# Kernel tuning notes

Hardware: AMD Instinct MI355X
Metric: run time of the kernel (lower is better)

The kernel has to match this reference:

```python
import jax, jax.numpy as jnp
import numpy as np

B, L, D = 2, 4096, 2048
H = 8
DK = D // H   # head qk dim = 256
DV = D // H   # head v dim = 256
KCONV = 4
BT = 64       # chunk size
EPS = 1e-5


def setup_inputs() -> dict:
    key = jax.random.key(0)
    ks = jax.random.split(key, 10)
    s = 0.02  # xavier-ish init scale (gain 2**-2.5)
    return {
        "hidden_states": jax.random.normal(ks[0], (B, L, D), jnp.float32),
        "Wq": jax.random.normal(ks[1], (D, D), jnp.float32) * s,
        "Wk": jax.random.normal(ks[2], (D, D), jnp.float32) * s,
        "Wv": jax.random.normal(ks[3], (D, D), jnp.float32) * s,
        "Wb": jax.random.normal(ks[4], (H, D), jnp.float32) * s,
        "conv_q": jax.random.normal(ks[5], (D, KCONV), jnp.float32) * 0.5,
        "conv_k": jax.random.normal(ks[6], (D, KCONV), jnp.float32) * 0.5,
        "conv_v": jax.random.normal(ks[7], (D, KCONV), jnp.float32) * 0.5,
        "g_norm": jnp.ones((DV,), jnp.float32),
        "Wo": jax.random.normal(ks[8], (D, D), jnp.float32) * s,
    }


def _causal_conv_silu(x, w):
    # depthwise causal conv1d (ShortConvolution), x: [B,L,C], w: [C,K]; silu activation
    K = w.shape[1]
    xp = jnp.pad(x, ((0, 0), (K - 1, 0), (0, 0)))
    Lx = x.shape[1]
    y = xp[:, 0:Lx, :] * w[:, 0]
    for j in range(1, K):
        y = y + xp[:, j:j + Lx, :] * w[:, j]
    return jax.nn.silu(y)


def _l2norm(x):
    return x * jax.lax.rsqrt(jnp.sum(x * x, -1, keepdims=True) + 1e-6)


def _chunk_delta_rule(q, k, v, beta):
    # q,k: [B,H,L,DK], v: [B,H,L,DV], beta: [B,H,L]
    b, h, Lq, dk = q.shape
    dv = v.shape[-1]
    nc = Lq // BT
    q = q * (dk ** -0.5)
    kb = k * beta[..., None]
    vb = v * beta[..., None]
    ch = lambda x: x.reshape(b, h, nc, BT, x.shape[-1])
    qc, kc, kbc, vbc = ch(q), ch(k), ch(kb), ch(vb)
    tri_s = jnp.tril(jnp.ones((BT, BT), bool), -1)  # strictly lower
    tri = jnp.tril(jnp.ones((BT, BT), bool))        # lower incl diag
    # M = strict_lower(K_beta K^T); T = (I+M)^{-1} via unit-lower triangular solve
    M = jnp.where(tri_s, jnp.einsum('bhntd,bhnsd->bhnts', kbc, kc), 0.0)
    Lmat = jnp.eye(BT, dtype=q.dtype) + M
    W = jax.scipy.linalg.solve_triangular(Lmat, kbc, lower=True, unit_diagonal=True)  # T @ k_beta
    U = jax.scipy.linalg.solve_triangular(Lmat, vbc, lower=True, unit_diagonal=True)  # T @ v_beta

    def step(S, xs):
        q_i, k_i, w_i, u_i = xs  # each [b,h,BT,d]
        attn = jnp.where(tri, jnp.einsum('bhtd,bhsd->bhts', q_i, k_i), 0.0)
        u_new = u_i - jnp.einsum('bhtd,bhdv->bhtv', w_i, S)
        o_i = jnp.einsum('bhtd,bhdv->bhtv', q_i, S) + jnp.einsum('bhts,bhsv->bhtv', attn, u_new)
        S = S + jnp.einsum('bhtd,bhtv->bhdv', k_i, u_new)
        return S, o_i

    mv = lambda x: jnp.moveaxis(x, 2, 0)  # chunk axis to front for scan
    S0 = jnp.zeros((b, h, dk, dv), q.dtype)
    S, o = jax.lax.scan(step, S0, (mv(qc), mv(kc), mv(W), mv(U)))
    o = jnp.moveaxis(o, 0, 2).reshape(b, h, Lq, dv)
    return o, S


def reference(hidden_states, Wq, Wk, Wv, Wb, conv_q, conv_k, conv_v, g_norm, Wo):
    hs = hidden_states
    q = _causal_conv_silu(hs @ Wq.T, conv_q)
    k = _causal_conv_silu(hs @ Wk.T, conv_k)
    v = _causal_conv_silu(hs @ Wv.T, conv_v)
    tohead = lambda x: x.reshape(B, L, H, -1).transpose(0, 2, 1, 3)  # b l (h d) -> b h l d
    q, k, v = tohead(q), tohead(k), tohead(v)
    q, k = _l2norm(q), _l2norm(k)
    beta = jax.nn.sigmoid(hs @ Wb.T).transpose(0, 2, 1)  # [B,H,L]
    o, _ = _chunk_delta_rule(q, k, v, beta)
    o = o.transpose(0, 2, 1, 3)  # [B,L,H,DV]
    o = o * jax.lax.rsqrt(jnp.mean(o * o, -1, keepdims=True) + EPS) * g_norm  # per-head RMSNorm
    return o.reshape(B, L, D) @ Wo.T
```

## Files before the change

kernel.cpp:

```cpp
#include <hip/hip_runtime.h>
#include <stdint.h>

#define TOK    8192
#define LDIM   4096
#define DDIM   2048
#define NBH    16
#define DK     256
#define NCHUNK 64

typedef __attribute__((ext_vector_type(8))) short bf16x8;
typedef __attribute__((ext_vector_type(4))) float f32x4;

#define MFMA(a,b,c) __builtin_amdgcn_mfma_f32_16x16x32_bf16((a),(b),(c),0,0,0)

__device__ __forceinline__ unsigned short f2bf(float f){
  union { float f; uint32_t u; } v; v.f = f;
  uint32_t r = v.u + 0x7FFFu + ((v.u >> 16) & 1u);
  return (unsigned short)(r >> 16);
}
__device__ __forceinline__ float bf2f(unsigned short u){
  union { uint32_t u; float f; } v; v.u = ((uint32_t)u) << 16;
  return v.f;
}

typedef __attribute__((address_space(1))) unsigned int as1_u32;
typedef __attribute__((address_space(3))) unsigned int as3_u32;
__device__ __forceinline__ void gload16(const void* g, void* l){
  __builtin_amdgcn_global_load_lds((const as1_u32*)g, (as3_u32*)l, 16, 0, 0);
}

__global__ void k_guard(float* o){ if (threadIdx.x == 0) o[0] = 0.f; }

__global__ __launch_bounds__(256) void k_f2bf(const float* __restrict__ s,
                                              unsigned short* __restrict__ d, int n)
{
  int i = (blockIdx.x*256 + threadIdx.x)*4;
  if (i >= n) return;
  float4 v = *(const float4*)(s + i);
  ushort4 o; o.x=f2bf(v.x); o.y=f2bf(v.y); o.z=f2bf(v.z); o.w=f2bf(v.w);
  *(ushort4*)(d + i) = o;
}

__global__ __launch_bounds__(256) void k_beta(const float* __restrict__ hs,
                                              const float* __restrict__ Wb,
                                              float* __restrict__ beta)
{
  const long t = blockIdx.x;
  const int tid = threadIdx.x;
  float acc[8] = {0,0,0,0,0,0,0,0};
  const float* xr = hs + t*DDIM;
  for (int i = tid; i < DDIM; i += 256){
    float x = xr[i];
    #pragma unroll
    for (int h=0; h<8; h++) acc[h] += x * Wb[h*DDIM + i];
  }
  __shared__ float red[8][4];
  const int w = tid >> 6, lane = tid & 63;
  #pragma unroll
  for (int h=0; h<8; h++){
    float s = acc[h];
    #pragma unroll
    for (int off=32; off; off>>=1) s += __shfl_down(s, off, 64);
    if (lane == 0) red[h][w] = s;
  }
  __syncthreads();
  if (tid < 8){
    float s = red[tid][0]+red[tid][1]+red[tid][2]+red[tid][3];
    float bv = 1.f/(1.f + __expf(-s));
    int b = (int)(t >> 12), l = (int)(t & 4095);
    beta[((long)(b*8 + tid))*LDIM + l] = bv;
  }
}

template <bool F32OUT>
__global__ __launch_bounds__(256,2) void k_gemm_bt(
    const unsigned short* __restrict__ A, const unsigned short* __restrict__ Bw,
    void* __restrict__ Cv, int M, int N, int K)
{
  __shared__ unsigned short As[128*32];
  __shared__ unsigned short Bs[128*32];
  const int tid = threadIdx.x;
  const int w = tid >> 6, l = tid & 63;
  const int lo = l & 15, quad = l >> 4;
  const int wm = w >> 1, wn = w & 1;
  const int gx = gridDim.x;
  int id = blockIdx.y * gx + blockIdx.x;
  const int nwg = gx * gridDim.y;
  if ((nwg & 7) == 0){
    const int q8 = nwg >> 3;
    id = (id & 7) * q8 + (id >> 3);
  }
  const int bx = id % gx, by = id / gx;
  const long tm = (long)by * 128, tn = (long)bx * 128;
  const int slot0 = (w*2+0)*64 + l;
  const int slot1 = (w*2+1)*64 + l;
  const int r0 = slot0 >> 2, c0 = (slot0 & 3) * 8;
  const int r1 = slot1 >> 2, c1 = (slot1 & 3) * 8;
  const unsigned short* pA0 = A  + (tm + r0)*(long)K + c0;
  const unsigned short* pA1 = A  + (tm + r1)*(long)K + c1;
  const unsigned short* pB0 = Bw + (tn + r0)*(long)K + c0;
  const unsigned short* pB1 = Bw + (tn + r1)*(long)K + c1;
  unsigned short* lA0 = &As[slot0*8]; unsigned short* lA1 = &As[slot1*8];
  unsigned short* lB0 = &Bs[slot0*8]; unsigned short* lB1 = &Bs[slot1*8];
  f32x4 acc[4][4] = {};
  for (int k0 = 0; k0 < K; k0 += 32){
    __syncthreads();
    gload16(pA0 + k0, lA0);
    gload16(pA1 + k0, lA1);
    gload16(pB0 + k0, lB0);
    gload16(pB1 + k0, lB1);
    __syncthreads();
    bf16x8 af[4], bg[4];
    #pragma unroll
    for (int i=0;i<4;i++){
      af[i] = *(const bf16x8*)&As[(wm*64 + i*16 + lo)*32 + quad*8];
      bg[i] = *(const bf16x8*)&Bs[(wn*64 + i*16 + lo)*32 + quad*8];
    }
    #pragma unroll
    for (int mt=0; mt<4; mt++)
      #pragma unroll
      for (int nt=0; nt<4; nt++)
        acc[mt][nt] = MFMA(af[mt], bg[nt], acc[mt][nt]);
  }
  #pragma unroll
  for (int mt=0; mt<4; mt++)
    #pragma unroll
    for (int nt=0; nt<4; nt++)
      #pragma unroll
      for (int r=0; r<4; r++){
        long m = tm + wm*64 + mt*16 + quad*4 + r;
        long n = tn + wn*64 + nt*16 + lo;
        if (F32OUT) ((float*)Cv)[m*N + n] = acc[mt][nt][r];
        else ((unsigned short*)Cv)[m*N + n] = f2bf(acc[mt][nt][r]);
      }
}

__global__ __launch_bounds__(256) void k_conv(
  const unsigned short* __restrict__ X, const float* __restrict__ Wc,
  const float* __restrict__ beta,
  unsigned short* __restrict__ O, int mode)
{
  const int lt = blockIdx.x, bh = blockIdx.y;
  const int b = bh >> 3, h = bh & 7;
  const int d = threadIdx.x;
  const int ch = h*256 + d;
  const int l0 = lt*64;
  const unsigned short* xp = X + (long)b*LDIM*DDIM + ch;
  const float4 wv = *(const float4*)(Wc + ch*4);
  float x0=0.f, x1=0.f, x2=0.f;
  if (l0 >= 3){
    x0 = bf2f(xp[(long)(l0-3)*DDIM]);
    x1 = bf2f(xp[(long)(l0-2)*DDIM]);
    x2 = bf2f(xp[(long)(l0-1)*DDIM]);
  }
  float y[64];
  #pragma unroll
  for (int i=0;i<64;i++){
    float x3 = bf2f(xp[(long)(l0+i)*DDIM]);
    float s = x0*wv.x + x1*wv.y + x2*wv.z + x3*wv.w;
    y[i] = s / (1.f + __expf(-s));
    x0 = x1; x1 = x2; x2 = x3;
  }
  unsigned short* op = O + (long)bh*LDIM*DK + d;
  if (mode == 2){
    const float* bet = beta + (long)bh*LDIM + l0;
    #pragma unroll
    for (int i=0;i<64;i++) op[(long)(l0+i)*DK] = f2bf(y[i]*bet[i]);
    return;
  }
  __shared__ float red[64*4];
  __shared__ float scl[64];
  const int wv_i = threadIdx.x >> 6, lane = threadIdx.x & 63;
  #pragma unroll
  for (int i=0;i<64;i++){
    float ss = y[i]*y[i];
    #pragma unroll
    for (int off=32; off; off>>=1) ss += __shfl_down(ss, off, 64);
    if (lane == 0) red[i*4 + wv_i] = ss;
  }
  __syncthreads();
  if (threadIdx.x < 64){
    int i = threadIdx.x;
    float s = red[i*4]+red[i*4+1]+red[i*4+2]+red[i*4+3];
    scl[i] = rsqrtf(s + 1e-6f) * (mode==0 ? 0.0625f : 1.f);
  }
  __syncthreads();
  #pragma unroll
  for (int i=0;i<64;i++) op[(long)(l0+i)*DK] = f2bf(y[i]*scl[i]);
}

__global__ __launch_bounds__(256) void k_transpose(
  const unsigned short* __restrict__ kH, unsigned short* __restrict__ kT)
{
  const int lt = blockIdx.x, dt = blockIdx.y, bh = blockIdx.z;
  __shared__ unsigned short tk[64][72];
  const int tid = threadIdx.x;
  const int rl = tid >> 2, c0 = (tid & 3) * 16;
  const long base = ((long)bh*LDIM + lt*64 + rl)*DK + dt*64 + c0;
  *(bf16x8*)&tk[rl][c0]   = *(const bf16x8*)(kH + base);
  *(bf16x8*)&tk[rl][c0+8] = *(const bf16x8*)(kH + base + 8);
  __syncthreads();
  const int rd = tid >> 2, lc0 = (tid & 3) * 16;
  bf16x8 ok0, ok1;
  #pragma unroll
  for (int j=0;j<16;j++){
    unsigned short kraw = tk[lc0+j][rd];
    if (j < 8) ok0[j] = (short)kraw; else ok1[j-8] = (short)kraw;
  }
  const long ob = ((long)bh*DK + dt*64 + rd)*LDIM + lt*64 + lc0;
  *(bf16x8*)(kT + ob) = ok0; *(bf16x8*)(kT + ob + 8) = ok1;
}

__global__ __launch_bounds__(256) void k_passA(
  const unsigned short* __restrict__ qH, const unsigned short* __restrict__ kH,
  const unsigned short* vbH,
  const unsigned short* __restrict__ kT,
  const float* __restrict__ beta,
  unsigned short* Wout,
  unsigned short* __restrict__ Uout,
  unsigned short* __restrict__ Aout)
{
  const int c = blockIdx.x, bh = blockIdx.y;
  __shared__ unsigned short Nn[64*72];
  __shared__ unsigned short NT[64*72];
  __shared__ unsigned short Pb[64*72];
  __shared__ unsigned short vT[256*72];
  const int tid = threadIdx.x;
  const int w = tid >> 6, l = tid & 63, lo = l & 15, quad = l >> 4;
  const long tokBase = (long)bh*LDIM + c*64;
  const unsigned short* qrow = qH + tokBase*DK;
  const unsigned short* krow = kH + tokBase*DK;
  const float bv = beta[tokBase + w*16 + lo];

  {
    const int r = tid >> 2, cs = (tid & 3) * 64;
    const unsigned short* vrow = vbH + (tokBase + r)*DK + cs;
    bf16x8 vv[8];
    #pragma unroll
    for (int j=0;j<8;j++) vv[j] = *(const bf16x8*)(vrow + j*8);
    #pragma unroll
    for (int j=0;j<8;j++)
      #pragma unroll
      for (int e=0;e<8;e++)
        vT[(cs + j*8 + e)*72 + r] = (unsigned short)vv[j][e];
  }

  f32x4 mAcc[4] = {}; f32x4 aAcc[4] = {};
  #pragma unroll
  for (int ks=0; ks<8; ks++){
    bf16x8 kf[4];
    #pragma unroll
    for (int nt=0; nt<4; nt++)
      kf[nt] = *(const bf16x8*)&krow[(nt*16+lo)*DK + ks*32 + quad*8];
    bf16x8 qf  = *(const bf16x8*)&qrow[(w*16+lo)*DK + ks*32 + quad*8];
    bf16x8 kfw = *(const bf16x8*)&krow[(w*16+lo)*DK + ks*32 + quad*8];
    bf16x8 kbf;
    #pragma unroll
    for (int j=0;j<8;j++) kbf[j] = (short)f2bf(bf2f((unsigned short)kfw[j]) * bv);
    #pragma unroll
    for (int nt=0; nt<4; nt++){
      mAcc[nt] = MFMA(kbf, kf[nt], mAcc[nt]);
      aAcc[nt] = MFMA(qf,  kf[nt], aAcc[nt]);
    }
  }
  unsigned short* Ap = Aout + ((long)bh*NCHUNK + c)*64*64;
  #pragma unroll
  for (int nt=0; nt<4; nt++)
    #pragma unroll
    for (int r=0; r<4; r++){
      int t = w*16 + quad*4 + r, s = nt*16 + lo;
      float mv = (t > s) ? mAcc[nt][r] : 0.f;
      unsigned short mb = f2bf(mv);
      Nn[t*72+s] = mb;
      NT[s*72+t] = mb;
      Pb[t*72+s] = f2bf((t==s ? 1.f : 0.f) - mv);
      Ap[t*64+s] = f2bf((t >= s) ? aAcc[nt][r] : 0.f);
    }
  __syncthreads();

  #pragma unroll 1
  for (int it=0; it<5; it++){
    bf16x8 aN[2], aP[2], bN[2][4];
    #pragma unroll
    for (int ks=0; ks<2; ks++){
      aN[ks] = *(const bf16x8*)&Nn[(w*16+lo)*72 + ks*32 + quad*8];
      aP[ks] = *(const bf16x8*)&Pb[(w*16+lo)*72 + ks*32 + quad*8];
      #pragma unroll
      for (int nt=0; nt<4; nt++)
        bN[ks][nt] = *(const bf16x8*)&NT[(nt*16+lo)*72 + ks*32 + quad*8];
    }
    f32x4 pp[4];
    #pragma unroll
    for (int nt=0; nt<4; nt++)
      #pragma unroll
      for (int r=0; r<4; r++)
        pp[nt][r] = bf2f(Pb[(w*16+quad*4+r)*72 + nt*16+lo]);
    __syncthreads();
    f32x4 sq[4] = {};
    #pragma unroll
    for (int ks=0; ks<2; ks++)
      #pragma unroll
      for (int nt=0; nt<4; nt++)
        sq[nt] = MFMA(aN[ks], bN[ks][nt], sq[nt]);
    #pragma unroll
    for (int nt=0; nt<4; nt++)
      #pragma unroll
      for (int r=0; r<4; r++){
        int t = w*16 + quad*4 + r, s = nt*16 + lo;
        unsigned short vb2 = f2bf(sq[nt][r]);
        Nn[t*72+s] = vb2; NT[s*72+t] = vb2;
      }
    __syncthreads();
    #pragma unroll
    for (int ks=0; ks<2; ks++)
      #pragma unroll
      for (int nt=0; nt<4; nt++){
        bf16x8 b = *(const bf16x8*)&NT[(nt*16+lo)*72 + ks*32 + quad*8];
        pp[nt] = MFMA(aP[ks], b, pp[nt]);
      }
    #pragma unroll
    for (int nt=0; nt<4; nt++)
      #pragma unroll
      for (int r=0; r<4; r++)
        Pb[(w*16+quad*4+r)*72 + nt*16+lo] = f2bf(pp[nt][r]);
    __syncthreads();
  }

  float b8[2][8];
  #pragma unroll
  for (int ks=0; ks<2; ks++)
    #pragma unroll
    for (int e=0; e<8; e++)
      b8[ks][e] = beta[tokBase + ks*32 + quad*8 + e];
  const unsigned short* kTb = kT + (long)bh*DK*LDIM + c*64;
  unsigned short* Wp = Wout + tokBase*DK;
  unsigned short* Up = Uout + tokBase*DK;
  #pragma unroll 1
  for (int nl=0; nl<4; nl++){
    const int d = (w*4 + nl)*16 + lo;
    f32x4 wa[4] = {}; f32x4 ua[4] = {};
    #pragma unroll
    for (int ks=0; ks<2; ks++){
      bf16x8 braw = *(const bf16x8*)&kTb[(long)d*LDIM + ks*32 + quad*8];
      bf16x8 bw;
      #pragma unroll
      for (int e=0; e<8; e++) bw[e] = (short)f2bf(bf2f((unsigned short)braw[e]) * b8[ks][e]);
      bf16x8 bu = *(const bf16x8*)&vT[d*72 + ks*32 + quad*8];
      #pragma unroll
      for (int mt=0; mt<4; mt++){
        bf16x8 a = *(const bf16x8*)&Pb[(mt*16+lo)*72 + ks*32 + quad*8];
        wa[mt] = MFMA(a, bw, wa[mt]);
        ua[mt] = MFMA(a, bu, ua[mt]);
      }
    }
    #pragma unroll
    for (int mt=0; mt<4; mt++)
      #pragma unroll
      for (int r=0; r<4; r++){
        int t = mt*16 + quad*4 + r;
        Wp[t*DK + d] = f2bf(wa[mt][r]);
        Up[t*DK + d] = f2bf(ua[mt][r]);
      }
  }
}

__device__ __forceinline__ int sidx(int n, int d){
  return n*256 + (((d>>3) ^ (n&7))<<3) + (d&7);
}
__device__ __forceinline__ int uidx(int n, int t){
  return n*64 + ((((t>>3) ^ (n&7)) & 7)<<3) + (t&7);
}

struct PrefWU {
  bf16x8 wf[8];
  unsigned short uf[8];
};

__device__ __forceinline__ void load_wu(PrefWU& P,
    const unsigned short* __restrict__ Wp, const unsigned short* __restrict__ Up,
    int c, int w, int lo, int quad, int vb)
{
  const unsigned short* Wc = Wp + (long)c*64*DK;
  const unsigned short* Uc = Up + (long)c*64*DK;
  #pragma unroll
  for (int ks=0; ks<8; ks++)
    P.wf[ks] = *(const bf16x8*)&Wc[(w*16+lo)*DK + ks*32 + quad*8];
  const int t0 = w*16 + quad*4;
  #pragma unroll
  for (int nt=0; nt<2; nt++)
    #pragma unroll
    for (int r=0; r<4; r++)
      P.uf[nt*4+r] = Uc[(t0+r)*DK + vb*32 + nt*16 + lo];
}

__device__ __forceinline__ void scan_chunk(const PrefWU& P, int c,
  const unsigned short* __restrict__ qp, const unsigned short* __restrict__ kTp,
  const unsigned short* __restrict__ Ap, unsigned short* __restrict__ op,
  unsigned short* S_l, unsigned short* u_l, f32x4 (&S)[4][2],
  int w, int lo, int quad, int vb)
{
  const unsigned short* qc = qp + (long)c*64*DK;
  const unsigned short* Ac = Ap + (long)c*64*64;
  bf16x8 qf[8], af[2], kf[4][2];
  #pragma unroll
  for (int ks=0; ks<8; ks++)
    qf[ks] = *(const bf16x8*)&qc[(w*16+lo)*DK + ks*32 + quad*8];
  #pragma unroll
  for (int ks=0; ks<2; ks++)
    af[ks] = *(const bf16x8*)&Ac[(w*16+lo)*64 + ks*32 + quad*8];
  #pragma unroll
  for (int mtl=0; mtl<4; mtl++)
    #pragma unroll
    for (int ks=0; ks<2; ks++)
      kf[mtl][ks] = *(const bf16x8*)&kTp[(long)(w*64+mtl*16+lo)*LDIM + c*64 + ks*32 + quad*8];

  f32x4 ua[2] = {};
  #pragma unroll
  for (int ks=0; ks<8; ks++)
    #pragma unroll
    for (int nt=0; nt<2; nt++){
      bf16x8 b = *(const bf16x8*)&S_l[sidx(nt*16+lo, ks*32+quad*8)];
      ua[nt] = MFMA(P.wf[ks], b, ua[nt]);
    }
  {
    const int t0 = w*16 + quad*4;
    #pragma unroll
    for (int nt=0; nt<2; nt++){
      const int n = nt*16 + lo;
      ushort4 pk;
      pk.x = f2bf(bf2f(P.uf[nt*4+0]) - ua[nt][0]);
      pk.y = f2bf(bf2f(P.uf[nt*4+1]) - ua[nt][1]);
      pk.z = f2bf(bf2f(P.uf[nt*4+2]) - ua[nt][2]);
      pk.w = f2bf(bf2f(P.uf[nt*4+3]) - ua[nt][3]);
      *(ushort4*)&u_l[uidx(n, t0)] = pk;
    }
  }
  __syncthreads();
  f32x4 oa[2] = {};
  #pragma unroll
  for (int ks=0; ks<8; ks++)
    #pragma unroll
    for (int nt=0; nt<2; nt++){
      bf16x8 b = *(const bf16x8*)&S_l[sidx(nt*16+lo, ks*32+quad*8)];
      oa[nt] = MFMA(qf[ks], b, oa[nt]);
    }
  #pragma unroll
  for (int ks=0; ks<2; ks++)
    #pragma unroll
    for (int nt=0; nt<2; nt++){
      bf16x8 b = *(const bf16x8*)&u_l[uidx(nt*16+lo, ks*32+quad*8)];
      oa[nt] = MFMA(af[ks], b, oa[nt]);
    }
  #pragma unroll
  for (int nt=0; nt<2; nt++)
    #pragma unroll
    for (int r=0; r<4; r++)
      op[(long)(c*64 + w*16 + quad*4 + r)*DK + vb*32 + nt*16 + lo] = f2bf(oa[nt][r]);
  #pragma unroll
  for (int mtl=0; mtl<4; mtl++)
    #pragma unroll
    for (int ks=0; ks<2; ks++)
      #pragma unroll
      for (int nt=0; nt<2; nt++){
        bf16x8 b = *(const bf16x8*)&u_l[uidx(nt*16+lo, ks*32+quad*8)];
        S[mtl][nt] = MFMA(kf[mtl][ks], b, S[mtl][nt]);
      }
  __syncthreads();
  #pragma unroll
  for (int mtl=0; mtl<4; mtl++)
    #pragma unroll
    for (int nt=0; nt<2; nt++){
      const int n = nt*16 + lo;
      const int d0 = w*64 + mtl*16 + quad*4;
      ushort4 pk;
      pk.x = f2bf(S[mtl][nt][0]); pk.y = f2bf(S[mtl][nt][1]);
      pk.z = f2bf(S[mtl][nt][2]); pk.w = f2bf(S[mtl][nt][3]);
      *(ushort4*)&S_l[sidx(n, d0)] = pk;
    }
  __syncthreads();
}

__global__ __launch_bounds__(256,1) void k_scan(
  const unsigned short* __restrict__ Wm, const unsigned short* __restrict__ Um,
  const unsigned short* __restrict__ qH, const unsigned short* __restrict__ kT,
  const unsigned short* __restrict__ Abuf, unsigned short* __restrict__ oH)
{
  const int bh = blockIdx.x, vb = blockIdx.y;
  __shared__ unsigned short S_l[32*256];
  __shared__ unsigned short u_l[32*64];
  const int tid = threadIdx.x;
  const int w = tid >> 6, l = tid & 63, lo = l & 15, quad = l >> 4;
  for (int i = tid; i < 2048; i += 256) ((unsigned long long*)S_l)[i] = 0ULL;
  f32x4 S[4][2] = {};
  const long hb = (long)bh * LDIM;
  const unsigned short* Wp = Wm + hb*DK;
  const unsigned short* Up = Um + hb*DK;
  const unsigned short* qp = qH + hb*DK;
  const unsigned short* kTp = kT + (long)bh*DK*LDIM;
  const unsigned short* Ap = Abuf + (long)bh*NCHUNK*64*64;
  unsigned short* op = oH + hb*DK;
  PrefWU PA, PB;
  load_wu(PA, Wp, Up, 0, w, lo, quad, vb);
  __syncthreads();
  #pragma unroll 1
  for (int c = 0; c < NCHUNK; c += 2){
    load_wu(PB, Wp, Up, c+1, w, lo, quad, vb);
    scan_chunk(PA, c,   qp, kTp, Ap, op, S_l, u_l, S, w, lo, quad, vb);
    load_wu(PA, Wp, Up, (c+2 < NCHUNK) ? c+2 : NCHUNK-1, w, lo, quad, vb);
    scan_chunk(PB, c+1, qp, kTp, Ap, op, S_l, u_l, S, w, lo, quad, vb);
  }
}

__global__ __launch_bounds__(64) void k_rms(
  const unsigned short* __restrict__ oH, const float* __restrict__ g,
  unsigned short* __restrict__ oN)
{
  const int ln = blockIdx.x, bh = blockIdx.y;
  const int b = bh >> 3, h = bh & 7;
  ushort4 u = *(const ushort4*)(oH + ((long)bh*LDIM + ln)*DK + threadIdx.x*4);
  float4 v; v.x = bf2f(u.x); v.y = bf2f(u.y); v.z = bf2f(u.z); v.w = bf2f(u.w);
  float ss = v.x*v.x + v.y*v.y + v.z*v.z + v.w*v.w;
  #pragma unroll
  for (int off=32; off; off>>=1) ss += __shfl_down(ss, off, 64);
  ss = __shfl(ss, 0, 64);
  const float sc = rsqrtf(ss*(1.f/DK) + 1e-5f);
  const float4 gv = *(const float4*)(g + threadIdx.x*4);
  unsigned short* o = oN + ((long)b*LDIM + ln)*DDIM + h*DK + threadIdx.x*4;
  ushort4 pk; pk.x=f2bf(v.x*sc*gv.x); pk.y=f2bf(v.y*sc*gv.y);
  pk.z=f2bf(v.z*sc*gv.z); pk.w=f2bf(v.w*sc*gv.w);
  *(ushort4*)o = pk;
}

extern "C" void kernel_launch(void* const* d_in, const int* in_sizes, int n_in,
                              void* d_out, int out_size, void* d_ws, size_t ws_size,
                              hipStream_t stream)
{
  (void)in_sizes; (void)n_in; (void)out_size;
  const float* hs = (const float*)d_in[0];
  const float* Wq = (const float*)d_in[1];
  const float* Wk = (const float*)d_in[2];
  const float* Wv = (const float*)d_in[3];
  const float* Wb = (const float*)d_in[4];
  const float* cq = (const float*)d_in[5];
  const float* ck = (const float*)d_in[6];
  const float* cv = (const float*)d_in[7];
  const float* gn = (const float*)d_in[8];
  const float* Wo = (const float*)d_in[9];

  const size_t SZ_TD2 = (size_t)TOK*DDIM*2;
  const size_t SZ_DD2 = (size_t)DDIM*DDIM*2;
  const size_t NEED  = 5*SZ_TD2 + 2*SZ_DD2 + (size_t)NBH*LDIM*4;
  const size_t NEEDW = NEED + SZ_TD2;
  if (ws_size < NEED){ k_guard<<<1, 64, 0, stream>>>((float*)d_out); return; }

  char* p = (char*)d_ws;
  unsigned short* bufA = (unsigned short*)p;      p += SZ_TD2;
  unsigned short* bufB = (unsigned short*)p;      p += SZ_DD2;
  unsigned short* bufC = (unsigned short*)p;      p += SZ_TD2;
  unsigned short* bufD = (unsigned short*)p;      p += SZ_TD2;
  unsigned short* bufE = (unsigned short*)p;      p += SZ_TD2;
  unsigned short* bufF = (unsigned short*)p;      p += SZ_TD2;
  unsigned short* bufG = (unsigned short*)p;      p += SZ_DD2;
  float*          beta = (float*)p;               p += (size_t)NBH*LDIM*4;
  unsigned short* bufW = (ws_size >= NEEDW) ? (unsigned short*)p : bufF;

  const dim3 gg(DDIM/128, TOK/128);
  const dim3 cg(LDIM/64, NBH);
  const int nTD = TOK*DDIM, nDD = DDIM*DDIM;

  k_f2bf<<<dim3(nTD/1024), 256, 0, stream>>>(hs, bufA, nTD);
  k_beta<<<dim3(TOK), 256, 0, stream>>>(hs, Wb, beta);

  k_f2bf<<<dim3(nDD/1024), 256, 0, stream>>>(Wq, bufB, nDD);
  k_gemm_bt<false><<<gg, 256, 0, stream>>>(bufA, bufB, bufC, TOK, DDIM, DDIM);
  k_conv<<<cg, 256, 0, stream>>>(bufC, cq, beta, bufD, 0);

  k_f2bf<<<dim3(nDD/1024), 256, 0, stream>>>(Wk, bufB, nDD);
  k_gemm_bt<false><<<gg, 256, 0, stream>>>(bufA, bufB, bufC, TOK, DDIM, DDIM);
  k_conv<<<cg, 256, 0, stream>>>(bufC, ck, beta, bufE, 1);

  k_f2bf<<<dim3(nDD/1024), 256, 0, stream>>>(Wv, bufB, nDD);
  k_gemm_bt<false><<<gg, 256, 0, stream>>>(bufA, bufB, bufC, TOK, DDIM, DDIM);
  k_conv<<<cg, 256, 0, stream>>>(bufC, cv, beta, bufF, 2);

  k_transpose<<<dim3(LDIM/64, DK/64, NBH), 256, 0, stream>>>(bufE, bufC);
  k_passA<<<dim3(NCHUNK, NBH), 256, 0, stream>>>(bufD, bufE, bufF, bufC, beta,
                                                 bufW, bufA , bufG);
  k_scan<<<dim3(NBH, 8), 256, 0, stream>>>(bufW, bufA, bufD, bufC, bufG, bufE);
  k_rms<<<dim3(LDIM, NBH), 64, 0, stream>>>(bufE, gn, bufC);

  k_f2bf<<<dim3(nDD/1024), 256, 0, stream>>>(Wo, bufB, nDD);
  k_gemm_bt<true><<<gg, 256, 0, stream>>>(bufC, bufB, d_out , TOK, DDIM, DDIM);
}
```

Before: 956.4 us.

## Double-buffer scan state in LDS and use chunk-major transposed K layout

The scan kernel's shared state matrix is now double-buffered, so each chunk reads the previous state from one buffer and writes the updated state to the other. This removes one block barrier per chunk and lets the q·S and w·S MFMAs share a single pass over the state reads. The transposed-K buffer is also relaid out chunk-major ([bh][chunk][d][64]), so each chunk's K^T slice is contiguous for both passA and the scan. The cost is twice the LDS for the state buffer and a layout dependency shared across three kernels.

```diff
diff --git a/kernel.cpp b/kernel.cpp
--- a/kernel.cpp
+++ b/kernel.cpp
@@ -207,7 +207,7 @@
     unsigned short kraw = tk[lc0+j][rd];
     if (j < 8) ok0[j] = (short)kraw; else ok1[j-8] = (short)kraw;
   }
-  const long ob = ((long)bh*DK + dt*64 + rd)*LDIM + lt*64 + lc0;
+  const long ob = (((long)bh*NCHUNK + lt)*DK + dt*64 + rd)*64 + lc0;
   *(bf16x8*)(kT + ob) = ok0; *(bf16x8*)(kT + ob + 8) = ok1;
 }
 
@@ -332,7 +332,7 @@
     #pragma unroll
     for (int e=0; e<8; e++)
       b8[ks][e] = beta[tokBase + ks*32 + quad*8 + e];
-  const unsigned short* kTb = kT + (long)bh*DK*LDIM + c*64;
+  const unsigned short* kTb = kT + ((long)bh*NCHUNK + c)*DK*64;
   unsigned short* Wp = Wout + tokBase*DK;
   unsigned short* Up = Uout + tokBase*DK;
   #pragma unroll 1
@@ -341,7 +341,7 @@
     f32x4 wa[4] = {}; f32x4 ua[4] = {};
     #pragma unroll
     for (int ks=0; ks<2; ks++){
-      bf16x8 braw = *(const bf16x8*)&kTb[(long)d*LDIM + ks*32 + quad*8];
+      bf16x8 braw = *(const bf16x8*)&kTb[(long)d*64 + ks*32 + quad*8];
       bf16x8 bw;
       #pragma unroll
       for (int e=0; e<8; e++) bw[e] = (short)f2bf(bf2f((unsigned short)braw[e]) * b8[ks][e]);
@@ -396,11 +396,13 @@
 __device__ __forceinline__ void scan_chunk(const PrefWU& P, int c,
   const unsigned short* __restrict__ qp, const unsigned short* __restrict__ kTp,
   const unsigned short* __restrict__ Ap, unsigned short* __restrict__ op,
-  unsigned short* S_l, unsigned short* u_l, f32x4 (&S)[4][2],
+  const unsigned short* __restrict__ Srd, unsigned short* __restrict__ Swr,
+  unsigned short* __restrict__ u_l, f32x4 (&S)[4][2],
   int w, int lo, int quad, int vb)
 {
   const unsigned short* qc = qp + (long)c*64*DK;
   const unsigned short* Ac = Ap + (long)c*64*64;
+  const unsigned short* kc = kTp + (long)c*DK*64;
   bf16x8 qf[8], af[2], kf[4][2];
   #pragma unroll
   for (int ks=0; ks<8; ks++)
@@ -412,15 +414,16 @@
   for (int mtl=0; mtl<4; mtl++)
     #pragma unroll
     for (int ks=0; ks<2; ks++)
-      kf[mtl][ks] = *(const bf16x8*)&kTp[(long)(w*64+mtl*16+lo)*LDIM + c*64 + ks*32 + quad*8];
-
-  f32x4 ua[2] = {};
+      kf[mtl][ks] = *(const bf16x8*)&kc[(w*64+mtl*16+lo)*64 + ks*32 + quad*8];
+
+  f32x4 ua[2] = {}; f32x4 oa[2] = {};
   #pragma unroll
   for (int ks=0; ks<8; ks++)
     #pragma unroll
     for (int nt=0; nt<2; nt++){
-      bf16x8 b = *(const bf16x8*)&S_l[sidx(nt*16+lo, ks*32+quad*8)];
+      bf16x8 b = *(const bf16x8*)&Srd[sidx(nt*16+lo, ks*32+quad*8)];
       ua[nt] = MFMA(P.wf[ks], b, ua[nt]);
+      oa[nt] = MFMA(qf[ks],  b, oa[nt]);
     }
   {
     const int t0 = w*16 + quad*4;
@@ -436,14 +439,6 @@
     }
   }
   __syncthreads();
-  f32x4 oa[2] = {};
-  #pragma unroll
-  for (int ks=0; ks<8; ks++)
-    #pragma unroll
-    for (int nt=0; nt<2; nt++){
-      bf16x8 b = *(const bf16x8*)&S_l[sidx(nt*16+lo, ks*32+quad*8)];
-      oa[nt] = MFMA(qf[ks], b, oa[nt]);
-    }
   #pragma unroll
   for (int ks=0; ks<2; ks++)
     #pragma unroll
@@ -465,7 +460,6 @@
         bf16x8 b = *(const bf16x8*)&u_l[uidx(nt*16+lo, ks*32+quad*8)];
         S[mtl][nt] = MFMA(kf[mtl][ks], b, S[mtl][nt]);
       }
-  __syncthreads();
   #pragma unroll
   for (int mtl=0; mtl<4; mtl++)
     #pragma unroll
@@ -475,7 +469,7 @@
       ushort4 pk;
       pk.x = f2bf(S[mtl][nt][0]); pk.y = f2bf(S[mtl][nt][1]);
       pk.z = f2bf(S[mtl][nt][2]); pk.w = f2bf(S[mtl][nt][3]);
-      *(ushort4*)&S_l[sidx(n, d0)] = pk;
+      *(ushort4*)&Swr[sidx(n, d0)] = pk;
     }
   __syncthreads();
 }
@@ -486,17 +480,17 @@
   const unsigned short* __restrict__ Abuf, unsigned short* __restrict__ oH)
 {
   const int bh = blockIdx.x, vb = blockIdx.y;
-  __shared__ unsigned short S_l[32*256];
+  __shared__ unsigned short S_l[2][32*256];
   __shared__ unsigned short u_l[32*64];
   const int tid = threadIdx.x;
   const int w = tid >> 6, l = tid & 63, lo = l & 15, quad = l >> 4;
-  for (int i = tid; i < 2048; i += 256) ((unsigned long long*)S_l)[i] = 0ULL;
+  for (int i = tid; i < 2048; i += 256) ((unsigned long long*)S_l[0])[i] = 0ULL;
   f32x4 S[4][2] = {};
   const long hb = (long)bh * LDIM;
   const unsigned short* Wp = Wm + hb*DK;
   const unsigned short* Up = Um + hb*DK;
   const unsigned short* qp = qH + hb*DK;
-  const unsigned short* kTp = kT + (long)bh*DK*LDIM;
+  const unsigned short* kTp = kT + (long)bh*NCHUNK*DK*64;
   const unsigned short* Ap = Abuf + (long)bh*NCHUNK*64*64;
   unsigned short* op = oH + hb*DK;
   PrefWU PA, PB;
@@ -505,9 +499,9 @@
   #pragma unroll 1
   for (int c = 0; c < NCHUNK; c += 2){
     load_wu(PB, Wp, Up, c+1, w, lo, quad, vb);
-    scan_chunk(PA, c,   qp, kTp, Ap, op, S_l, u_l, S, w, lo, quad, vb);
+    scan_chunk(PA, c,   qp, kTp, Ap, op, S_l[0], S_l[1], u_l, S, w, lo, quad, vb);
     load_wu(PA, Wp, Up, (c+2 < NCHUNK) ? c+2 : NCHUNK-1, w, lo, quad, vb);
-    scan_chunk(PB, c+1, qp, kTp, Ap, op, S_l, u_l, S, w, lo, quad, vb);
+    scan_chunk(PB, c+1, qp, kTp, Ap, op, S_l[1], S_l[0], u_l, S, w, lo, quad, vb);
   }
 }
 
```

After: 945.6 us. No clear change (-1.1%).
